# Performance work log

Hardware: AMD Instinct MI355X
Metric: run time of the kernel (lower is better)

The kernel has to match this reference:

```python
import jax, jax.numpy as jnp
import numpy as np
from jax import lax

THRESHOLD = 10.0  # p-norm threshold in HSEM
BN_EPS = 1e-5
DN = ('NCHW', 'OIHW', 'NCHW')


def setup_inputs() -> dict:
    key = jax.random.key(0)
    ks = jax.random.split(key, 9)
    b, c, h, w = 2, 256, 64, 64
    c_out = 512
    # scale x so pairwise L2 distances straddle the threshold (dense-ish hypergraph)
    x = jax.random.normal(ks[0], (b, c, h, w), dtype=jnp.float32) * 0.4
    fc_w = jax.random.normal(ks[1], (c, c), dtype=jnp.float32) * 0.02
    fc_b = jax.random.normal(ks[2], (c,), dtype=jnp.float32) * 0.02
    bn_gamma = jnp.ones((c,), dtype=jnp.float32)
    bn_beta = jnp.zeros((c,), dtype=jnp.float32)
    down_w = jax.random.normal(ks[3], (c, c, 3, 3), dtype=jnp.float32) * 0.02
    down_b = jax.random.normal(ks[4], (c,), dtype=jnp.float32) * 0.02
    out_w = jax.random.normal(ks[5], (c_out, c, 1, 1), dtype=jnp.float32) * 0.02
    out_b = jax.random.normal(ks[6], (c_out,), dtype=jnp.float32) * 0.02
    return {"x": x, "fc_w": fc_w, "fc_b": fc_b, "bn_gamma": bn_gamma,
            "bn_beta": bn_beta, "down_w": down_w, "down_b": down_b,
            "out_w": out_w, "out_b": out_b}


def _mean_agg(path, X):
    # path: [b, n_tgt, n_src], X: [b, n_src, d]; mean aggregation with inf->0 masking
    s = jnp.sum(path, axis=2, keepdims=True)           # [b, n_tgt, 1]
    norm = jnp.where(s > 0, 1.0 / jnp.where(s > 0, s, 1.0), 0.0)
    return norm * jnp.matmul(path, X)


def reference(x, fc_w, fc_b, bn_gamma, bn_beta, down_w, down_b, out_w, out_b):
    b, c, h, w = x.shape
    n = h * w
    xf = x.reshape(b, c, n).transpose(0, 2, 1)          # [b, n, c]
    # cdist (euclidean): ||a-b|| via expansion
    sq = jnp.sum(xf * xf, axis=-1)                      # [b, n]
    d2 = sq[:, :, None] + sq[:, None, :] - 2.0 * jnp.einsum('bnc,bmc->bnm', xf, xf)
    dist = jnp.sqrt(jnp.maximum(d2, 0.0))               # [b, n, n]
    hg = (dist < THRESHOLD).astype(x.dtype)             # dynamic hypergraph incidence
    # HyPConv: fc -> v2e (H^T) -> e2v (H)
    y = jnp.einsum('bnc,dc->bnd', xf, fc_w) + fc_b      # Linear(c1, c2)
    E = _mean_agg(jnp.swapaxes(hg, 1, 2), y)            # vertex -> edge
    v = _mean_agg(hg, E)                                # edge -> vertex
    xf = v + xf                                         # residual
    x4 = xf.transpose(0, 2, 1).reshape(b, c, h, w)
    # BatchNorm2d (training-mode batch statistics, biased var)
    mean = jnp.mean(x4, axis=(0, 2, 3))
    var = jnp.var(x4, axis=(0, 2, 3))
    xn = (x4 - mean[None, :, None, None]) * lax.rsqrt(var + BN_EPS)[None, :, None, None]
    xn = xn * bn_gamma[None, :, None, None] + bn_beta[None, :, None, None]
    xa = xn * jax.nn.sigmoid(xn)                        # SiLU
    # Downsample: pad (right=1, bottom=1) then 3x3 stride-2 VALID conv
    xp = jnp.pad(xa, ((0, 0), (0, 0), (0, 1), (0, 1)))
    xd = lax.conv_general_dilated(xp, down_w, (2, 2), 'VALID', dimension_numbers=DN)
    xd = xd + down_b[None, :, None, None]
    out = lax.conv_general_dilated(xd, out_w, (1, 1), 'VALID', dimension_numbers=DN)
    out = out + out_b[None, :, None, None]
    return out
```

## Files before the change

### kernel.cpp

```cpp
#include <hip/hip_runtime.h>
#include <hip/hip_bf16.h>
#include <math.h>

#define NPIX 4096
#define CH   256

#define OFF_XP    0u
#define OFF_XR    1048576u
#define OFF_VB    2097152u
#define OFF_TBS   3145728u
#define OFF_TBS2  4194304u
#define OFF_HG    5242880u
#define OFF_SQ    6291456u
#define OFF_PART  6299648u
#define OFF_BNSS  6365184u
#define OFF_DINV  6365696u
#define OFF_W3P   6373888u
#define OFF_WFCP  6668800u
#define OFF_WOUTP 6701568u

typedef __attribute__((ext_vector_type(8))) short bf16x8;
typedef __attribute__((ext_vector_type(16))) float f32x16;

static __device__ __forceinline__ short f2b(float f) {
  __hip_bfloat16 h = __float2bfloat16(f);
  return *reinterpret_cast<short*>(&h);
}
static __device__ __forceinline__ float b2f(short s) {
  union { unsigned u; float f; } r;
  r.u = ((unsigned)(unsigned short)s) << 16;
  return r.f;
}

static __device__ __forceinline__ bf16x8 byte2bf(unsigned byte) {
  union { unsigned u[4]; bf16x8 h; } r;
  r.u[0] = ((byte * 0x8001u) & 0x10001u) * 0x3F80u;
  r.u[1] = (((byte >> 2) * 0x8001u) & 0x10001u) * 0x3F80u;
  r.u[2] = (((byte >> 4) * 0x8001u) & 0x10001u) * 0x3F80u;
  r.u[3] = (((byte >> 6) * 0x8001u) & 0x10001u) * 0x3F80u;
  return r.h;
}

static __device__ __forceinline__ size_t packoff(int m, int c) {
  return ((size_t)((m >> 5) * 16 + (c >> 4)) * 2 + ((c >> 3) & 1)) * 256 + (m & 31) * 8 + (c & 7);
}

__global__ __launch_bounds__(256) void k_front2(const float* __restrict__ x,
                                                short* __restrict__ xp,
                                                float* __restrict__ sq,
                                                const float* __restrict__ fc_w,
                                                const float* __restrict__ ow,
                                                const float* __restrict__ dw,
                                                short* __restrict__ wfcp,
                                                short* __restrict__ woutp,
                                                short* __restrict__ w3p) {
  __shared__ float lds[256][33];
  __shared__ float red2[8][32];
  const int bid = blockIdx.x;
  const int t = threadIdx.x;
  if (bid < 256) {
    const int b = bid >> 7;
    const int n0 = (bid & 127) * 32;
    const float* xb = x + (size_t)b * CH * NPIX + n0;
    const int j = t & 31, cg8 = t >> 5;
#pragma unroll 4
    for (int it = 0; it < 32; ++it) {
      const int c = it * 8 + cg8;
      lds[c][j] = xb[(size_t)c * NPIX + j];
    }
    __syncthreads();
    {
      const int n = t & 31, cg = t >> 5;
      float s = 0.f;
#pragma unroll 8
      for (int i = 0; i < 32; ++i) {
        const float v = lds[cg * 32 + i][n];
        s += v * v;
      }
      red2[cg][n] = s;
    }
    short* xpb = xp + (size_t)b * NPIX * CH;
#pragma unroll
    for (int i = 0; i < 4; ++i) {
      const int f = i * 256 + t;
      const int n = f & 31, c0 = (f >> 5) * 8;
      short tmp[8];
#pragma unroll
      for (int k = 0; k < 8; ++k) tmp[k] = f2b(lds[c0 + k][n]);
      short* dst = xpb + packoff(n0 + n, c0);
      *(short4*)dst = *(short4*)&tmp[0];
      *(short4*)(dst + 4) = *(short4*)&tmp[4];
    }
    __syncthreads();
    if (t < 32) {
      float s = 0.f;
#pragma unroll
      for (int cg = 0; cg < 8; ++cg) s += red2[cg][t];
      sq[b * NPIX + n0 + t] = s;
    }
  } else {
    const int i = (bid - 256) * 256 + t;
    if (i < 65536) {
      wfcp[packoff(i >> 8, i & 255)] = f2b(fc_w[i]);
    } else if (i < 196608) {
      const int j = i - 65536;
      woutp[packoff(j >> 8, j & 255)] = f2b(ow[j]);
    } else {
      const int j = i - 196608;
      const int oc = j / 2304;
      const int rem = j % 2304;
      const int c = rem / 9, tap = rem % 9;
      const size_t off = ((size_t)((tap * 8 + (oc >> 5)) * 16 + (c >> 4)) * 2 + ((c >> 3) & 1)) * 256
                       + (oc & 31) * 8 + (c & 7);
      w3p[off] = f2b(dw[j]);
    }
  }
}

__global__ __launch_bounds__(256, 2) void k_gram3(const short* __restrict__ xp,
                                                  const float* __restrict__ sq,
                                                  unsigned* __restrict__ hgbit) {
  const int b = blockIdx.z;
  int tt = blockIdx.x;
  int bi = 0;
  while (true) { const int cnt = 16 - (bi >> 1); if (tt < cnt) break; tt -= cnt; ++bi; }
  const int bj = (bi >> 1) + tt;
  const int i0 = bi * 128, j0 = bj * 256;

  const int t = threadIdx.x;
  const int lane = t & 63, wid = t >> 6;
  const int wm = wid >> 1, wn = wid & 1;
  const int c = lane & 31, h = lane >> 5;
  const short* xb = xp + (size_t)b * NPIX * CH;
  const int ibase = i0 + wm * 64;
  const int jbase = j0 + wn * 128;

  f32x16 acc[2][4];
#pragma unroll
  for (int m = 0; m < 2; ++m)
#pragma unroll
    for (int n = 0; n < 4; ++n)
#pragma unroll
      for (int r = 0; r < 16; ++r) acc[m][n][r] = 0.f;

  const short* pa = xb + (size_t)(ibase >> 5) * 8192 + lane * 8;
  const short* pb = xb + (size_t)(jbase >> 5) * 8192 + lane * 8;

#pragma unroll 2
  for (int kb = 0; kb < 16; ++kb) {
    const bf16x8 a0 = *(const bf16x8*)(pa + kb * 512);
    const bf16x8 a1 = *(const bf16x8*)(pa + 8192 + kb * 512);
    bf16x8 bb[4];
#pragma unroll
    for (int n = 0; n < 4; ++n) bb[n] = *(const bf16x8*)(pb + (size_t)n * 8192 + kb * 512);
#pragma unroll
    for (int n = 0; n < 4; ++n) {
      acc[0][n] = __builtin_amdgcn_mfma_f32_32x32x16_bf16(a0, bb[n], acc[0][n], 0, 0, 0);
      acc[1][n] = __builtin_amdgcn_mfma_f32_32x32x16_bf16(a1, bb[n], acc[1][n], 0, 0, 0);
    }
  }

  const int sqb = b * NPIX;
#pragma unroll
  for (int m = 0; m < 2; ++m) {
    float4 sqa[4];
#pragma unroll
    for (int q = 0; q < 4; ++q)
      sqa[q] = *(const float4*)(sq + sqb + ibase + m * 32 + q * 8 + 4 * h);
#pragma unroll
    for (int n = 0; n < 4; ++n) {
      const float sj = sq[sqb + jbase + n * 32 + c];
      const int wj = (jbase + n * 32) >> 5;
#pragma unroll
      for (int q = 0; q < 4; ++q) {
        const float sqq[4] = {sqa[q].x, sqa[q].y, sqa[q].z, sqa[q].w};
#pragma unroll
        for (int rr = 0; rr < 4; ++rr) {
          const int reg = q * 4 + rr;
          const float d2 = sqq[rr] + sj - 2.f * acc[m][n][reg];
          const unsigned long long bal = __ballot(d2 < 100.f);
          if ((lane & 31) == reg) {
            const int row = ibase + m * 32 + rr + 8 * q + 4 * h;
            const unsigned wd = h ? (unsigned)(bal >> 32) : (unsigned)bal;
            hgbit[(size_t)(sqb + row) * 128 + wj] = wd;
          }
        }
      }
    }
  }
}

__global__ void k_mirror(unsigned* __restrict__ hg) {
  const int b = blockIdx.y;
  const int g = threadIdx.x >> 5;
  const int r = threadIdx.x & 31;
  const int tile = blockIdx.x * 8 + g;
  const int ta = tile >> 7, tb = tile & 127;
  if ((ta >> 2) <= (tb >> 2)) return;
  unsigned* H = hg + (size_t)b * NPIX * 128;
  unsigned w = H[(size_t)(tb * 32 + r) * 128 + ta];
#pragma unroll
  for (int s = 16; s >= 1; s >>= 1) {
    const unsigned M = (s == 16) ? 0xFFFF0000u : (s == 8) ? 0xFF00FF00u :
                       (s == 4) ? 0xF0F0F0F0u : (s == 2) ? 0xCCCCCCCCu : 0xAAAAAAAAu;
    const unsigned p = __shfl_xor(w, s, 32);
    w = (r & s) ? ((w & M) | ((p >> s) & ~M)) : ((w & ~M) | ((p << s) & M));
  }
  H[(size_t)(ta * 32 + r) * 128 + tb] = w;
}

__global__ __launch_bounds__(256) void k_fcdinv(const short* __restrict__ wfcp,
                                                const short* __restrict__ xp,
                                                short* __restrict__ C,
                                                const float* __restrict__ bias,
                                                const unsigned* __restrict__ hg,
                                                float* __restrict__ dinvf) {
  const int bid = blockIdx.x;
  const int t = threadIdx.x;
  if (bid >= 256) {
    const int row = (bid - 256) * 4 + (t >> 6);
    const int l = t & 63;
    const unsigned w0 = hg[(size_t)row * 128 + l * 2];
    const unsigned w1 = hg[(size_t)row * 128 + l * 2 + 1];
    int n = __popc(w0) + __popc(w1);
#pragma unroll
    for (int off = 32; off; off >>= 1) n += __shfl_down(n, off);
    if (l == 0) dinvf[row] = 1.0f / (float)n;
    return;
  }
  const int b = bid >> 7;
  const short* xpb = xp + (size_t)b * NPIX * CH;
  short* Cb = C + ((size_t)b << 20);
  const int l = t & 63, wid = t >> 6;
  const int m0 = ((bid >> 6) & 1) * 128 + wid * 32, n0 = (bid & 63) * 64;
  const int col = l & 31, half = l >> 5;
  f32x16 acc[2];
#pragma unroll
  for (int nt = 0; nt < 2; ++nt)
#pragma unroll
    for (int r = 0; r < 16; ++r) acc[nt][r] = 0.f;
  const short* pa = wfcp + (size_t)(m0 >> 5) * 8192 + l * 8;
  const short* pb = xpb + (size_t)(n0 >> 5) * 8192 + l * 8;
#pragma unroll 4
  for (int kb = 0; kb < 16; ++kb) {
    const bf16x8 a = *(const bf16x8*)(pa + kb * 512);
    const bf16x8 b0 = *(const bf16x8*)(pb + kb * 512);
    const bf16x8 b1 = *(const bf16x8*)(pb + 8192 + kb * 512);
    acc[0] = __builtin_amdgcn_mfma_f32_32x32x16_bf16(a, b0, acc[0], 0, 0, 0);
    acc[1] = __builtin_amdgcn_mfma_f32_32x32x16_bf16(a, b1, acc[1], 0, 0, 0);
  }
  const int cb = m0 >> 5;
#pragma unroll
  for (int nt = 0; nt < 2; ++nt) {
    const int node = n0 + nt * 32 + col;
    short* dst = Cb + ((size_t)cb * 512 + (node >> 3)) * 256 + (node & 7);
#pragma unroll
    for (int q = 0; q < 4; ++q)
#pragma unroll
      for (int rr = 0; rr < 4; ++rr) {
        const int c31 = rr + 8 * q + 4 * half;
        dst[c31 * 8] = f2b(acc[nt][q * 4 + rr] + bias[m0 + c31]);
      }
  }
}

__global__ __launch_bounds__(256) void k_hgemm_t4(const short* __restrict__ tbs,
                                                  const unsigned* __restrict__ hg,
                                                  const float* __restrict__ dinvf,
                                                  short* __restrict__ tbs2) {
  __shared__ float red[4][64][33];
  const int b = blockIdx.z;
  const int n0 = blockIdx.x * 64;
  const int cbp = blockIdx.y;
  const int ks = threadIdx.x >> 6;
  const int l = threadIdx.x & 63;
  const int col = l & 31, half = l >> 5;
  const int sh8 = half * 8;

  f32x16 acc00, acc01, acc10, acc11;
#pragma unroll
  for (int r = 0; r < 16; ++r) { acc00[r] = 0.f; acc01[r] = 0.f; acc10[r] = 0.f; acc11[r] = 0.f; }

  const short* pa0 = tbs + ((size_t)b << 20) + ((size_t)(cbp * 2) * 512 + half) * 256
                   + col * 8 + ks * 32768;
  const short* pa1 = pa0 + 131072;
  const uint4* hrow0 = (const uint4*)((const unsigned char*)hg
                     + ((size_t)b * NPIX + n0 + col) * 512 + ks * 128);
  const uint4* hrow1 = (const uint4*)((const unsigned char*)hg
                     + ((size_t)b * NPIX + n0 + 32 + col) * 512 + ks * 128);

#pragma unroll 2
  for (int o = 0; o < 8; ++o) {
    const uint4 wq0 = hrow0[o];
    const uint4 wq1 = hrow1[o];
    const unsigned ww0[4] = {wq0.x, wq0.y, wq0.z, wq0.w};
    const unsigned ww1[4] = {wq1.x, wq1.y, wq1.z, wq1.w};
#pragma unroll
    for (int s = 0; s < 4; ++s) {
      const bf16x8 a00 = *(const bf16x8*)(pa0);
      const bf16x8 a01 = *(const bf16x8*)(pa0 + 512);
      const bf16x8 a10 = *(const bf16x8*)(pa1);
      const bf16x8 a11 = *(const bf16x8*)(pa1 + 512);
      pa0 += 1024; pa1 += 1024;
      const bf16x8 b0 = byte2bf((ww0[s] >> sh8) & 0xFFu);
      const bf16x8 b1 = byte2bf((ww0[s] >> (16 + sh8)) & 0xFFu);
      const bf16x8 c0 = byte2bf((ww1[s] >> sh8) & 0xFFu);
      const bf16x8 c1 = byte2bf((ww1[s] >> (16 + sh8)) & 0xFFu);
      acc00 = __builtin_amdgcn_mfma_f32_32x32x16_bf16(a00, b0, acc00, 0, 0, 0);
      acc00 = __builtin_amdgcn_mfma_f32_32x32x16_bf16(a01, b1, acc00, 0, 0, 0);
      acc10 = __builtin_amdgcn_mfma_f32_32x32x16_bf16(a10, b0, acc10, 0, 0, 0);
      acc10 = __builtin_amdgcn_mfma_f32_32x32x16_bf16(a11, b1, acc10, 0, 0, 0);
      acc01 = __builtin_amdgcn_mfma_f32_32x32x16_bf16(a00, c0, acc01, 0, 0, 0);
      acc01 = __builtin_amdgcn_mfma_f32_32x32x16_bf16(a01, c1, acc01, 0, 0, 0);
      acc11 = __builtin_amdgcn_mfma_f32_32x32x16_bf16(a10, c0, acc11, 0, 0, 0);
      acc11 = __builtin_amdgcn_mfma_f32_32x32x16_bf16(a11, c1, acc11, 0, 0, 0);
    }
  }

#pragma unroll
  for (int r = 0; r < 16; ++r) { red[ks][l][r] = acc00[r]; red[ks][l][16 + r] = acc10[r]; }
  __syncthreads();
  {
    const int n = n0 + col;
    const float dinv = dinvf[b * NPIX + n];
    short* dst0 = tbs2 + ((size_t)b << 20) + ((size_t)(cbp * 2) * 512 + (n >> 3)) * 256 + (n & 7);
    short* dst1 = dst0 + 131072;
#pragma unroll
    for (int rj = 0; rj < 8; ++rj) {
      const int reg = ks * 8 + rj;
      const float s = red[0][l][reg] + red[1][l][reg] + red[2][l][reg] + red[3][l][reg];
      const int rm = reg & 15;
      const int c31 = (rm & 3) + 8 * (rm >> 2) + 4 * half;
      (reg < 16 ? dst0 : dst1)[c31 * 8] = f2b(s * dinv);
    }
  }
  __syncthreads();
#pragma unroll
  for (int r = 0; r < 16; ++r) { red[ks][l][r] = acc01[r]; red[ks][l][16 + r] = acc11[r]; }
  __syncthreads();
  {
    const int n = n0 + 32 + col;
    const float dinv = dinvf[b * NPIX + n];
    short* dst0 = tbs2 + ((size_t)b << 20) + ((size_t)(cbp * 2) * 512 + (n >> 3)) * 256 + (n & 7);
    short* dst1 = dst0 + 131072;
#pragma unroll
    for (int rj = 0; rj < 8; ++rj) {
      const int reg = ks * 8 + rj;
      const float s = red[0][l][reg] + red[1][l][reg] + red[2][l][reg] + red[3][l][reg];
      const int rm = reg & 15;
      const int c31 = (rm & 3) + 8 * (rm >> 2) + 4 * half;
      (reg < 16 ? dst0 : dst1)[c31 * 8] = f2b(s * dinv);
    }
  }
}

__global__ __launch_bounds__(256) void k_hgemm_n4(const unsigned* __restrict__ hg,
                                                  const short* __restrict__ tbs2,
                                                  const float* __restrict__ dinvf,
                                                  const short* __restrict__ xp,
                                                  short* __restrict__ vb) {
  __shared__ float red[4][64][33];
  const int b = blockIdx.z;
  const int cbp = blockIdx.x;
  const int m0 = blockIdx.y * 64;
  const int ks = threadIdx.x >> 6;
  const int l = threadIdx.x & 63;
  const int col = l & 31, half = l >> 5;
  const int sh8 = half * 8;

  f32x16 acc00, acc01, acc10, acc11;
#pragma unroll
  for (int r = 0; r < 16; ++r) { acc00[r] = 0.f; acc01[r] = 0.f; acc10[r] = 0.f; acc11[r] = 0.f; }

  const short* pb0 = tbs2 + ((size_t)b << 20) + ((size_t)(cbp * 2) * 512 + half) * 256
                   + col * 8 + ks * 32768;
  const short* pb1 = pb0 + 131072;
  const uint4* hrow0 = (const uint4*)((const unsigned char*)hg
                     + ((size_t)b * NPIX + m0 + col) * 512 + ks * 128);
  const uint4* hrow1 = (const uint4*)((const unsigned char*)hg
                     + ((size_t)b * NPIX + m0 + 32 + col) * 512 + ks * 128);

#pragma unroll 2
  for (int o = 0; o < 8; ++o) {
    const uint4 wq0 = hrow0[o];
    const uint4 wq1 = hrow1[o];
    const unsigned ww0[4] = {wq0.x, wq0.y, wq0.z, wq0.w};
    const unsigned ww1[4] = {wq1.x, wq1.y, wq1.z, wq1.w};
#pragma unroll
    for (int s = 0; s < 4; ++s) {
      const bf16x8 b00 = *(const bf16x8*)(pb0);
      const bf16x8 b01 = *(const bf16x8*)(pb0 + 512);
      const bf16x8 b10 = *(const bf16x8*)(pb1);
      const bf16x8 b11 = *(const bf16x8*)(pb1 + 512);
      pb0 += 1024; pb1 += 1024;
      const bf16x8 a0 = byte2bf((ww0[s] >> sh8) & 0xFFu);
      const bf16x8 a1 = byte2bf((ww0[s] >> (16 + sh8)) & 0xFFu);
      const bf16x8 a2 = byte2bf((ww1[s] >> sh8) & 0xFFu);
      const bf16x8 a3 = byte2bf((ww1[s] >> (16 + sh8)) & 0xFFu);
      acc00 = __builtin_amdgcn_mfma_f32_32x32x16_bf16(a0, b00, acc00, 0, 0, 0);
      acc00 = __builtin_amdgcn_mfma_f32_32x32x16_bf16(a1, b01, acc00, 0, 0, 0);
      acc01 = __builtin_amdgcn_mfma_f32_32x32x16_bf16(a0, b10, acc01, 0, 0, 0);
      acc01 = __builtin_amdgcn_mfma_f32_32x32x16_bf16(a1, b11, acc01, 0, 0, 0);
      acc10 = __builtin_amdgcn_mfma_f32_32x32x16_bf16(a2, b00, acc10, 0, 0, 0);
      acc10 = __builtin_amdgcn_mfma_f32_32x32x16_bf16(a3, b01, acc10, 0, 0, 0);
      acc11 = __builtin_amdgcn_mfma_f32_32x32x16_bf16(a2, b10, acc11, 0, 0, 0);
      acc11 = __builtin_amdgcn_mfma_f32_32x32x16_bf16(a3, b11, acc11, 0, 0, 0);
    }
  }

  const short* xpb = xp + (size_t)b * NPIX * CH;
#pragma unroll
  for (int r = 0; r < 16; ++r) { red[ks][l][r] = acc00[r]; red[ks][l][16 + r] = acc01[r]; }
  __syncthreads();
  {
    const int cc = cbp * 64 + col;
#pragma unroll
    for (int rj = 0; rj < 8; ++rj) {
      const int reg = ks * 8 + rj;
      const float s = red[0][l][reg] + red[1][l][reg] + red[2][l][reg] + red[3][l][reg];
      const int rm = reg & 15;
      const int r = m0 + (rm & 3) + 8 * (rm >> 2) + 4 * half;
      const int ccc = cc + (reg < 16 ? 0 : 32);
      const size_t o = ((size_t)(b * NPIX + r)) * CH + ccc;
      vb[o] = f2b(s * dinvf[b * NPIX + r] + b2f(xpb[packoff(r, ccc)]));
    }
  }
  __syncthreads();
#pragma unroll
  for (int r = 0; r < 16; ++r) { red[ks][l][r] = acc10[r]; red[ks][l][16 + r] = acc11[r]; }
  __syncthreads();
  {
    const int cc = cbp * 64 + col;
#pragma unroll
    for (int rj = 0; rj < 8; ++rj) {
      const int reg = ks * 8 + rj;
      const float s = red[0][l][reg] + red[1][l][reg] + red[2][l][reg] + red[3][l][reg];
      const int rm = reg & 15;
      const int r = m0 + 32 + (rm & 3) + 8 * (rm >> 2) + 4 * half;
      const int ccc = cc + (reg < 16 ? 0 : 32);
      const size_t o = ((size_t)(b * NPIX + r)) * CH + ccc;
      vb[o] = f2b(s * dinvf[b * NPIX + r] + b2f(xpb[packoff(r, ccc)]));
    }
  }
}

__global__ void k_bnstat(const short* __restrict__ vb, float* __restrict__ part) {
  const int t = threadIdx.x, blk = blockIdx.x;
  float s = 0.f, ss = 0.f;
  const short* p = vb + (size_t)blk * 64 * CH;
  for (int r = 0; r < 64; ++r) {
    const float v = b2f(p[r * CH + t]);
    s += v; ss += v * v;
  }
  part[blk * 512 + t] = s;
  part[blk * 512 + 256 + t] = ss;
}

__global__ void k_bnfin(const float* __restrict__ part, const float* __restrict__ gamma,
                        const float* __restrict__ beta, float* __restrict__ bnss) {
  const int t = threadIdx.x;
  float s = 0.f, ss = 0.f;
  for (int i = 0; i < 128; ++i) { s += part[i * 512 + t]; ss += part[i * 512 + 256 + t]; }
  const float mean = s * (1.f / 8192.f);
  const float var = ss * (1.f / 8192.f) - mean * mean;
  const float inv = rsqrtf(var + 1e-5f);
  const float sc = gamma[t] * inv;
  bnss[t] = sc;
  bnss[256 + t] = beta[t] - mean * sc;
}

__global__ void k_bnapply3(const short* __restrict__ vb, const float* __restrict__ bnss,
                           short* __restrict__ xpp) {
  const int i = blockIdx.x * 256 + threadIdx.x;
  const short4 sv = reinterpret_cast<const short4*>(vb)[i];
  const int c0 = (i & 63) * 4;
  const int n = (i >> 6) & 4095;
  const int b = i >> 18;
  const float4 sc = *(const float4*)(bnss + c0);
  const float4 sh = *(const float4*)(bnss + 256 + c0);
  const float u0 = b2f(sv.x) * sc.x + sh.x;
  const float u1 = b2f(sv.y) * sc.y + sh.y;
  const float u2 = b2f(sv.z) * sc.z + sh.z;
  const float u3 = b2f(sv.w) * sc.w + sh.w;
  short4 o;
  o.x = f2b(u0 / (1.f + expf(-u0)));
  o.y = f2b(u1 / (1.f + expf(-u1)));
  o.z = f2b(u2 / (1.f + expf(-u2)));
  o.w = f2b(u3 / (1.f + expf(-u3)));
  const int ih = n >> 6, iw = n & 63;
  const int p = iw & 1, ow = iw >> 1;
  const size_t off = ((size_t)(((b * 2 + p) * 64 + ih) * 16 + (c0 >> 4)) * 2 + ((c0 >> 3) & 1)) * 256
                   + ow * 8 + (c0 & 7);
  *(short4*)(xpp + off) = o;
}

__global__ __launch_bounds__(64) void k_conv5(const short* __restrict__ xpp,
                                              const short* __restrict__ w3p,
                                              float* __restrict__ convp) {
  const int ocg = blockIdx.x;
  const int oh = blockIdx.y;
  const int bz = blockIdx.z;
  const int b = bz & 1, cs = bz >> 1;
  const int l = threadIdx.x;
  const int col = l & 31;
  const bf16x8 zv = {0, 0, 0, 0, 0, 0, 0, 0};

  f32x16 acc;
#pragma unroll
  for (int r = 0; r < 16; ++r) acc[r] = 0.f;

  for (int kh = 0; kh < 3; ++kh) {
    const int ih = 2 * oh + kh;
    if (ih >= 64) continue;
#pragma unroll
    for (int kw = 0; kw < 3; ++kw) {
      const int p = kw & 1;
      const short* pa = xpp + ((size_t)((b * 2 + p) * 64 + ih) * 16 + cs * 4) * 512
                      + l * 8 + (kw == 2 ? 8 : 0);
      const short* pb = w3p + ((size_t)((kh * 3 + kw) * 8 + ocg) * 16 + cs * 4) * 512 + l * 8;
      const bool kill = (kw == 2) && (col == 31);
#pragma unroll
      for (int kb = 0; kb < 4; ++kb) {
        bf16x8 a = *(const bf16x8*)(pa + kb * 512);
        if (kill) a = zv;
        const bf16x8 bb = *(const bf16x8*)(pb + kb * 512);
        acc = __builtin_amdgcn_mfma_f32_32x32x16_bf16(a, bb, acc, 0, 0, 0);
      }
    }
  }
  const int half = l >> 5;
  const int oc = ocg * 32 + col;
#pragma unroll
  for (int q = 0; q < 4; ++q)
#pragma unroll
    for (int rr = 0; rr < 4; ++rr) {
      const int ow = rr + 8 * q + 4 * half;
      convp[((size_t)bz * 1024 + oh * 32 + ow) * 256 + oc] = acc[q * 4 + rr];
    }
}

__global__ void k_convmerge3(const float* __restrict__ convp, const float* __restrict__ db,
                             short* __restrict__ xdtb) {
  const int i = blockIdx.x * 256 + threadIdx.x;
  const int b = i >> 16, px = (i >> 6) & 1023, oc0 = (i & 63) * 4;
  const size_t base = ((size_t)px) * 256 + oc0;
  const float4 h0 = *(const float4*)(convp + ((size_t)(0 + b) << 18) + base);
  const float4 h1 = *(const float4*)(convp + ((size_t)(2 + b) << 18) + base);
  const float4 h2 = *(const float4*)(convp + ((size_t)(4 + b) << 18) + base);
  const float4 h3 = *(const float4*)(convp + ((size_t)(6 + b) << 18) + base);
  const float4 bv = *(const float4*)(db + oc0);
  short4 o;
  o.x = f2b(h0.x + h1.x + h2.x + h3.x + bv.x);
  o.y = f2b(h0.y + h1.y + h2.y + h3.y + bv.y);
  o.z = f2b(h0.z + h1.z + h2.z + h3.z + bv.z);
  o.w = f2b(h0.w + h1.w + h2.w + h3.w + bv.w);
  const size_t off = ((size_t)((b * 32 + (px >> 5)) * 16 + (oc0 >> 4)) * 2 + ((oc0 >> 3) & 1)) * 256
                   + (px & 31) * 8 + (oc0 & 7);
  *(short4*)(xdtb + off) = o;
}

__global__ __launch_bounds__(256) void k_mfma_nt2(const short* __restrict__ woutp,
                                                  const short* __restrict__ xdtb,
                                                  float* __restrict__ C,
                                                  const float* __restrict__ bias) {
  const int b = blockIdx.z;
  xdtb += (size_t)b * 1024 * CH;
  C += (size_t)b * 512 * 1024;
  const int t = threadIdx.x, l = t & 63, wid = t >> 6;
  const int m0 = blockIdx.y * 128 + wid * 32, n0 = blockIdx.x * 64;
  const int col = l & 31, half = l >> 5;
  f32x16 acc[2];
#pragma unroll
  for (int nt = 0; nt < 2; ++nt)
#pragma unroll
    for (int r = 0; r < 16; ++r) acc[nt][r] = 0.f;
  const short* pa = woutp + (size_t)(m0 >> 5) * 8192 + l * 8;
  const short* pb = xdtb + (size_t)(n0 >> 5) * 8192 + l * 8;
#pragma unroll 4
  for (int kb = 0; kb < 16; ++kb) {
    const bf16x8 a = *(const bf16x8*)(pa + kb * 512);
    const bf16x8 b0 = *(const bf16x8*)(pb + kb * 512);
    const bf16x8 b1 = *(const bf16x8*)(pb + 8192 + kb * 512);
    acc[0] = __builtin_amdgcn_mfma_f32_32x32x16_bf16(a, b0, acc[0], 0, 0, 0);
    acc[1] = __builtin_amdgcn_mfma_f32_32x32x16_bf16(a, b1, acc[1], 0, 0, 0);
  }
#pragma unroll
  for (int nt = 0; nt < 2; ++nt) {
#pragma unroll
    for (int q = 0; q < 4; ++q)
#pragma unroll
      for (int rr = 0; rr < 4; ++rr) {
        const int row = m0 + rr + 8 * q + 4 * half;
        const int cc = n0 + nt * 32 + col;
        C[(size_t)row * 1024 + cc] = acc[nt][q * 4 + rr] + bias[row];
      }
  }
}

extern "C" void kernel_launch(void* const* d_in, const int* in_sizes, int n_in,
                              void* d_out, int out_size, void* d_ws, size_t ws_size,
                              hipStream_t stream) {
  const float* x     = (const float*)d_in[0];
  const float* fc_w  = (const float*)d_in[1];
  const float* fc_b  = (const float*)d_in[2];
  const float* gamma = (const float*)d_in[3];
  const float* beta  = (const float*)d_in[4];
  const float* dw    = (const float*)d_in[5];
  const float* db    = (const float*)d_in[6];
  const float* ow    = (const float*)d_in[7];
  const float* ob    = (const float*)d_in[8];

  float* ws   = (float*)d_ws;
  short* xp   = (short*)(ws + OFF_XP);
  float* convp= ws + OFF_XP;
  short* vb   = (short*)(ws + OFF_VB);
  short* tbs  = (short*)(ws + OFF_TBS);
  short* xdtb = (short*)(ws + OFF_TBS);
  short* tbs2 = (short*)(ws + OFF_TBS2);
  short* xpp  = (short*)(ws + OFF_TBS2);
  unsigned* hg = (unsigned*)(ws + OFF_HG);
  float* sqv  = ws + OFF_SQ;
  float* part = ws + OFF_PART;
  float* bnss = ws + OFF_BNSS;
  float* dinvf= ws + OFF_DINV;
  short* w3p  = (short*)(ws + OFF_W3P);
  short* wfcp = (short*)(ws + OFF_WFCP);
  short* woutp= (short*)(ws + OFF_WOUTP);
  float* out  = (float*)d_out;

  k_front2<<<3328, 256, 0, stream>>>(x, xp, sqv, fc_w, ow, dw, wfcp, woutp, w3p);
  k_gram3<<<dim3(272, 1, 2), 256, 0, stream>>>(xp, sqv, hg);
  k_mirror<<<dim3(2048, 2), 256, 0, stream>>>(hg);
  k_fcdinv<<<2304, 256, 0, stream>>>(wfcp, xp, tbs, fc_b, hg, dinvf);
  k_hgemm_t4<<<dim3(64, 4, 2), 256, 0, stream>>>(tbs, hg, dinvf, tbs2);
  k_hgemm_n4<<<dim3(4, 64, 2), 256, 0, stream>>>(hg, tbs2, dinvf, xp, vb);
  k_bnstat<<<128, 256, 0, stream>>>(vb, part);
  k_bnfin<<<1, 256, 0, stream>>>(part, gamma, beta, bnss);
  k_bnapply3<<<2048, 256, 0, stream>>>(vb, bnss, xpp);
  k_conv5<<<dim3(8, 32, 8), 64, 0, stream>>>(xpp, w3p, convp);
  k_convmerge3<<<512, 256, 0, stream>>>(convp, db, xdtb);
  k_mfma_nt2<<<dim3(16, 4, 2), 256, 0, stream>>>(woutp, xdtb, out, ob);
}
```

Before: 134.3 us.

## Fuse hypergraph transpose into gram kernel and BN stats into hgemm

The gram kernel now uses square 128x128 upper-triangle tiles and writes both the bit-row and its transposed bit-column directly, which removes the separate mirror kernel. BatchNorm partial sums are accumulated with shared-memory atomics in the final hypergraph GEMM epilogue instead of a separate stats pass over vb. This saves two launches and one re-read of the activations. The cost is smaller blocks with more tiles, extra shuffles in the gram epilogue, and shared atomic contention in hgemm.

New measurement: 140.4 us. 1.05x slower.

```diff
diff --git a/kernel.cpp b/kernel.cpp
--- a/kernel.cpp
+++ b/kernel.cpp
@@ -117,23 +117,24 @@
   }
 }
 
-__global__ __launch_bounds__(256, 2) void k_gram3(const short* __restrict__ xp,
+__global__ __launch_bounds__(128, 2) void k_gram4(const short* __restrict__ xp,
                                                   const float* __restrict__ sq,
                                                   unsigned* __restrict__ hgbit) {
   const int b = blockIdx.z;
   int tt = blockIdx.x;
-  int bi = 0;
-  while (true) { const int cnt = 16 - (bi >> 1); if (tt < cnt) break; tt -= cnt; ++bi; }
-  const int bj = (bi >> 1) + tt;
-  const int i0 = bi * 128, j0 = bj * 256;
+  int bi = (int)((65.0f - sqrtf(4225.0f - 8.0f * (float)tt)) * 0.5f);
+  bi = bi < 0 ? 0 : (bi > 31 ? 31 : bi);
+  while (bi * (65 - bi) / 2 > tt) --bi;
+  while ((bi + 1) * (64 - bi) / 2 <= tt) ++bi;
+  const int bj = bi + (tt - bi * (65 - bi) / 2);
+  const int i0 = bi * 128, j0 = bj * 128;
 
   const int t = threadIdx.x;
-  const int lane = t & 63, wid = t >> 6;
-  const int wm = wid >> 1, wn = wid & 1;
+  const int lane = t & 63, w = t >> 6;
   const int c = lane & 31, h = lane >> 5;
   const short* xb = xp + (size_t)b * NPIX * CH;
-  const int ibase = i0 + wm * 64;
-  const int jbase = j0 + wn * 128;
+  const int ibase = i0 + w * 64;
+  const int jbase = j0;
 
   f32x16 acc[2][4];
 #pragma unroll
@@ -171,6 +172,7 @@
     for (int n = 0; n < 4; ++n) {
       const float sj = sq[sqb + jbase + n * 32 + c];
       const int wj = (jbase + n * 32) >> 5;
+      unsigned mmask = 0u;
 #pragma unroll
       for (int q = 0; q < 4; ++q) {
         const float sqq[4] = {sqa[q].x, sqa[q].y, sqa[q].z, sqa[q].w};
@@ -178,35 +180,23 @@
         for (int rr = 0; rr < 4; ++rr) {
           const int reg = q * 4 + rr;
           const float d2 = sqq[rr] + sj - 2.f * acc[m][n][reg];
-          const unsigned long long bal = __ballot(d2 < 100.f);
+          const bool cond = d2 < 100.f;
+          const unsigned long long bal = __ballot(cond);
           if ((lane & 31) == reg) {
             const int row = ibase + m * 32 + rr + 8 * q + 4 * h;
             const unsigned wd = h ? (unsigned)(bal >> 32) : (unsigned)bal;
             hgbit[(size_t)(sqb + row) * 128 + wj] = wd;
           }
+          mmask |= (cond ? 1u : 0u) << (rr + 8 * q + 4 * h);
         }
       }
-    }
-  }
-}
-
-__global__ void k_mirror(unsigned* __restrict__ hg) {
-  const int b = blockIdx.y;
-  const int g = threadIdx.x >> 5;
-  const int r = threadIdx.x & 31;
-  const int tile = blockIdx.x * 8 + g;
-  const int ta = tile >> 7, tb = tile & 127;
-  if ((ta >> 2) <= (tb >> 2)) return;
-  unsigned* H = hg + (size_t)b * NPIX * 128;
-  unsigned w = H[(size_t)(tb * 32 + r) * 128 + ta];
-#pragma unroll
-  for (int s = 16; s >= 1; s >>= 1) {
-    const unsigned M = (s == 16) ? 0xFFFF0000u : (s == 8) ? 0xFF00FF00u :
-                       (s == 4) ? 0xF0F0F0F0u : (s == 2) ? 0xCCCCCCCCu : 0xAAAAAAAAu;
-    const unsigned p = __shfl_xor(w, s, 32);
-    w = (r & s) ? ((w & M) | ((p >> s) & ~M)) : ((w & ~M) | ((p << s) & M));
-  }
-  H[(size_t)(ta * 32 + r) * 128 + tb] = w;
+      const unsigned merged = mmask | (unsigned)__shfl_xor((int)mmask, 32, 64);
+      if (h == 0) {
+        const int colg = jbase + n * 32 + c;
+        hgbit[(size_t)(sqb + colg) * 128 + ((ibase + m * 32) >> 5)] = merged;
+      }
+    }
+  }
 }
 
 __global__ __launch_bounds__(256) void k_fcdinv(const short* __restrict__ wfcp,
@@ -358,8 +348,10 @@
                                                   const short* __restrict__ tbs2,
                                                   const float* __restrict__ dinvf,
                                                   const short* __restrict__ xp,
-                                                  short* __restrict__ vb) {
+                                                  short* __restrict__ vb,
+                                                  float* __restrict__ part) {
   __shared__ float red[4][64][33];
+  __shared__ float bnp[128];
   const int b = blockIdx.z;
   const int cbp = blockIdx.x;
   const int m0 = blockIdx.y * 64;
@@ -367,6 +359,7 @@
   const int l = threadIdx.x & 63;
   const int col = l & 31, half = l >> 5;
   const int sh8 = half * 8;
+  if (threadIdx.x < 128) bnp[threadIdx.x] = 0.f;
 
   f32x16 acc00, acc01, acc10, acc11;
 #pragma unroll
@@ -422,7 +415,12 @@
       const int r = m0 + (rm & 3) + 8 * (rm >> 2) + 4 * half;
       const int ccc = cc + (reg < 16 ? 0 : 32);
       const size_t o = ((size_t)(b * NPIX + r)) * CH + ccc;
-      vb[o] = f2b(s * dinvf[b * NPIX + r] + b2f(xpb[packoff(r, ccc)]));
+      const short sv = f2b(s * dinvf[b * NPIX + r] + b2f(xpb[packoff(r, ccc)]));
+      vb[o] = sv;
+      const float vr = b2f(sv);
+      const int ci = col + (reg < 16 ? 0 : 32);
+      atomicAdd(&bnp[ci], vr);
+      atomicAdd(&bnp[64 + ci], vr * vr);
     }
   }
   __syncthreads();
@@ -439,28 +437,31 @@
       const int r = m0 + 32 + (rm & 3) + 8 * (rm >> 2) + 4 * half;
       const int ccc = cc + (reg < 16 ? 0 : 32);
       const size_t o = ((size_t)(b * NPIX + r)) * CH + ccc;
-      vb[o] = f2b(s * dinvf[b * NPIX + r] + b2f(xpb[packoff(r, ccc)]));
-    }
-  }
-}
-
-__global__ void k_bnstat(const short* __restrict__ vb, float* __restrict__ part) {
-  const int t = threadIdx.x, blk = blockIdx.x;
-  float s = 0.f, ss = 0.f;
-  const short* p = vb + (size_t)blk * 64 * CH;
-  for (int r = 0; r < 64; ++r) {
-    const float v = b2f(p[r * CH + t]);
-    s += v; ss += v * v;
-  }
-  part[blk * 512 + t] = s;
-  part[blk * 512 + 256 + t] = ss;
+      const short sv = f2b(s * dinvf[b * NPIX + r] + b2f(xpb[packoff(r, ccc)]));
+      vb[o] = sv;
+      const float vr = b2f(sv);
+      const int ci = col + (reg < 16 ? 0 : 32);
+      atomicAdd(&bnp[ci], vr);
+      atomicAdd(&bnp[64 + ci], vr * vr);
+    }
+  }
+  __syncthreads();
+  if (threadIdx.x < 128) {
+    const int slot = b * 64 + blockIdx.y;
+    part[((size_t)(cbp * 128 + slot)) * 128 + threadIdx.x] = bnp[threadIdx.x];
+  }
 }
 
 __global__ void k_bnfin(const float* __restrict__ part, const float* __restrict__ gamma,
                         const float* __restrict__ beta, float* __restrict__ bnss) {
   const int t = threadIdx.x;
+  const int cbp = t >> 6, ch = t & 63;
   float s = 0.f, ss = 0.f;
-  for (int i = 0; i < 128; ++i) { s += part[i * 512 + t]; ss += part[i * 512 + 256 + t]; }
+  for (int i = 0; i < 128; ++i) {
+    const float* p = part + ((size_t)(cbp * 128 + i)) * 128;
+    s += p[ch];
+    ss += p[64 + ch];
+  }
   const float mean = s * (1.f / 8192.f);
   const float var = ss * (1.f / 8192.f) - mean * mean;
   const float inv = rsqrtf(var + 1e-5f);
@@ -629,12 +630,10 @@
   float* out  = (float*)d_out;
 
   k_front2<<<3328, 256, 0, stream>>>(x, xp, sqv, fc_w, ow, dw, wfcp, woutp, w3p);
-  k_gram3<<<dim3(272, 1, 2), 256, 0, stream>>>(xp, sqv, hg);
-  k_mirror<<<dim3(2048, 2), 256, 0, stream>>>(hg);
+  k_gram4<<<dim3(528, 1, 2), 128, 0, stream>>>(xp, sqv, hg);
   k_fcdinv<<<2304, 256, 0, stream>>>(wfcp, xp, tbs, fc_b, hg, dinvf);
   k_hgemm_t4<<<dim3(64, 4, 2), 256, 0, stream>>>(tbs, hg, dinvf, tbs2);
-  k_hgemm_n4<<<dim3(4, 64, 2), 256, 0, stream>>>(hg, tbs2, dinvf, xp, vb);
-  k_bnstat<<<128, 256, 0, stream>>>(vb, part);
+  k_hgemm_n4<<<dim3(4, 64, 2), 256, 0, stream>>>(hg, tbs2, dinvf, xp, vb, part);
   k_bnfin<<<1, 256, 0, stream>>>(part, gamma, beta, bnss);
   k_bnapply3<<<2048, 256, 0, stream>>>(vb, bnss, xpp);
   k_conv5<<<dim3(8, 32, 8), 64, 0, stream>>>(xpp, w3p, convp);
```
